# Kernel optimization log

Hardware: AMD Instinct MI355X
Metric: run time of the kernel (lower is better)

Reference implementation:

```python
import jax, jax.numpy as jnp
import numpy as np

DIM = 768
NUM_EXPERTS = 1536
EXPERT_DIM = 64
NOISE_SCALE = 0.1
B, H, W = 1, 64, 64
N = B * H * W


def setup_inputs() -> dict:
    key = jax.random.key(0)
    ks = jax.random.split(key, 6)
    scaled = lambda k, shape, fan_in: (jax.random.normal(k, shape, jnp.float32) / np.sqrt(fan_in)).astype(jnp.float32)
    return {
        "x": jax.random.normal(ks[0], (B, H, W, DIM), jnp.float32),
        "noise": jax.random.normal(ks[1], (N, NUM_EXPERTS), jnp.float32),
        "gate_w": scaled(ks[2], (NUM_EXPERTS, DIM), DIM),
        "gate_b": jnp.zeros((NUM_EXPERTS,), jnp.float32),
        "expert_w": scaled(ks[3], (NUM_EXPERTS, EXPERT_DIM, DIM), DIM),  # torch Linear weight layout (out, in)
        "expert_b": jnp.zeros((NUM_EXPERTS, EXPERT_DIM), jnp.float32),
        "proj_w": scaled(ks[4], (DIM, EXPERT_DIM), EXPERT_DIM),
        "proj_b": jnp.zeros((DIM,), jnp.float32),
    }


def reference(x, noise, gate_w, gate_b, expert_w, expert_b, proj_w, proj_b):
    orig_shape = x.shape
    xf = x.reshape(-1, orig_shape[-1])  # (N, DIM)
    # Noisy gating
    scores = xf @ gate_w.T + gate_b + noise * NOISE_SCALE  # (N, E)
    gate_weights = jax.nn.softmax(scores, axis=-1)
    top_w, top_i = jax.lax.top_k(gate_weights, 1)  # (N, 1), (N, 1)
    idx = top_i[:, 0]  # (N,)
    # Gather only the selected expert per token (same math as the redundant
    # dense all-expert compute followed by a gather in the original).
    w_sel = expert_w[idx]  # (N, EXPERT_DIM, DIM)
    b_sel = expert_b[idx]  # (N, EXPERT_DIM)
    y = jnp.einsum('nd,nod->no', xf, w_sel) + b_sel  # (N, EXPERT_DIM)
    out_flat = (y @ proj_w.T + proj_b) * top_w  # (N, DIM); top_w broadcasts (N,1)
    return out_flat.reshape(orig_shape)
```

## Files before the change

### kernel.cpp

```cpp
#include <hip/hip_runtime.h>
#include <hip/hip_bf16.h>

#define NT 4096
#define DIM 768
#define NE 1536
#define ED 64
#define GAP_THR 8e-3f

typedef __attribute__((ext_vector_type(8))) short short8v;
typedef __attribute__((ext_vector_type(4))) float f32x4;

__device__ __forceinline__ unsigned short f2bf(float f) {
  unsigned int u = __float_as_uint(f);
  unsigned int r = (u + 0x7fffu + ((u >> 16) & 1u)) >> 16;
  return (unsigned short)r;
}
__device__ __forceinline__ float bf2f(unsigned short h) {
  return __uint_as_float(((unsigned int)h) << 16);
}

__device__ __forceinline__ void gload16(const void* g, void* l) {
  __builtin_amdgcn_global_load_lds((const __attribute__((address_space(1))) void*)g,
                                   (__attribute__((address_space(3))) void*)l, 16, 0, 0);
}

__global__ __launch_bounds__(256) void split_bf16(
    const float* __restrict__ src, unsigned short* __restrict__ hi,
    unsigned short* __restrict__ lo, int n4) {
  int i = blockIdx.x * 256 + threadIdx.x;
  if (i >= n4) return;
  float4 v = ((const float4*)src)[i];
  unsigned short h0 = f2bf(v.x), h1 = f2bf(v.y), h2 = f2bf(v.z), h3 = f2bf(v.w);
  ushort4 hv = make_ushort4(h0, h1, h2, h3);
  ushort4 lv = make_ushort4(f2bf(v.x - bf2f(h0)), f2bf(v.y - bf2f(h1)),
                            f2bf(v.z - bf2f(h2)), f2bf(v.w - bf2f(h3)));
  ((ushort4*)hi)[i] = hv;
  ((ushort4*)lo)[i] = lv;
}

__global__ __launch_bounds__(256) void gate_mfma(
    const unsigned short* __restrict__ xhi, const unsigned short* __restrict__ xlo,
    const unsigned short* __restrict__ ghi, const unsigned short* __restrict__ glo,
    const float* __restrict__ gb, const float* __restrict__ noise,
    float* __restrict__ scores) {
  __shared__ __align__(16) unsigned short sA[2 * 128 * 32];
  __shared__ __align__(16) unsigned short sB[2 * 128 * 32];
  const int tid = threadIdx.x;
  const int w = tid >> 6, lane = tid & 63;
  const int wr = w >> 1, wc = w & 1;
  const int bm = blockIdx.x, bn = blockIdx.y;
  const int fr = lane & 15;
  const int fg = lane >> 4;
  const int gsw = fg ^ ((fr >> 1) & 3);

  f32x4 acc[4][4];
#pragma unroll
  for (int i = 0; i < 4; i++)
#pragma unroll
    for (int j = 0; j < 4; j++) acc[i][j] = (f32x4){0.f, 0.f, 0.f, 0.f};

  const size_t arow = (size_t)bm * 128 * DIM;
  const size_t brow = (size_t)bn * 128 * DIM;
  const int sr_lo = tid >> 2;
  const int sg = (tid & 3) ^ ((tid >> 3) & 3);

  for (int kt = 0; kt < DIM; kt += 32) {
    __syncthreads();
#pragma unroll
    for (int h = 0; h < 2; h++) {
      const int r = h * 64 + sr_lo;
      const size_t asrc = arow + (size_t)r * DIM + kt + sg * 8;
      const size_t bsrc = brow + (size_t)r * DIM + kt + sg * 8;
      const int dofs = h * 2048 + w * 512;
      gload16(xhi + asrc, &sA[dofs]);
      gload16(xlo + asrc, &sA[4096 + dofs]);
      gload16(ghi + bsrc, &sB[dofs]);
      gload16(glo + bsrc, &sB[4096 + dofs]);
    }
    __syncthreads();

    short8v ah[4], al[4], bh[4], bl[4];
#pragma unroll
    for (int mf = 0; mf < 4; mf++) {
      int ro = (wr * 64 + mf * 16 + fr) * 32 + gsw * 8;
      ah[mf] = *(const short8v*)&sA[ro];
      al[mf] = *(const short8v*)&sA[4096 + ro];
    }
#pragma unroll
    for (int nf = 0; nf < 4; nf++) {
      int ro = (wc * 64 + nf * 16 + fr) * 32 + gsw * 8;
      bh[nf] = *(const short8v*)&sB[ro];
      bl[nf] = *(const short8v*)&sB[4096 + ro];
    }
#pragma unroll
    for (int mf = 0; mf < 4; mf++)
#pragma unroll
      for (int nf = 0; nf < 4; nf++) {
        f32x4 c = acc[mf][nf];
        c = __builtin_amdgcn_mfma_f32_16x16x32_bf16(ah[mf], bh[nf], c, 0, 0, 0);
        c = __builtin_amdgcn_mfma_f32_16x16x32_bf16(ah[mf], bl[nf], c, 0, 0, 0);
        c = __builtin_amdgcn_mfma_f32_16x16x32_bf16(al[mf], bh[nf], c, 0, 0, 0);
        acc[mf][nf] = c;
      }
  }

  const int gm0 = bm * 128 + wr * 64;
  const int gn0 = bn * 128 + wc * 64;
#pragma unroll
  for (int nf = 0; nf < 4; nf++) {
    const int gn = gn0 + nf * 16 + fr;
    const float gbv = gb[gn];
#pragma unroll
    for (int mf = 0; mf < 4; mf++) {
      const int gmb = gm0 + mf * 16 + fg * 4;
#pragma unroll
      for (int reg = 0; reg < 4; reg++) {
        const size_t o = (size_t)(gmb + reg) * NE + gn;
        scores[o] = acc[mf][nf][reg] + gbv + 0.1f * noise[o];
      }
    }
  }
}

__global__ __launch_bounds__(256) void softmax_top1(
    const float* __restrict__ scores, float* __restrict__ topw,
    int* __restrict__ idx, int* __restrict__ rc_count,
    int* __restrict__ rc_n, int* __restrict__ rc_i2) {
  const int widx = threadIdx.x >> 6;
  const int lane = threadIdx.x & 63;
  const int n = blockIdx.x * 4 + widx;
  const float* s = scores + (size_t)n * NE;

  float v[24];
  float m1 = -1e30f, m2 = -1e30f;
  int i1 = 0, i2 = 0;
#pragma unroll
  for (int j = 0; j < 24; j++) {
    int ii = lane + 64 * j;
    v[j] = s[ii];
    if (v[j] > m1) { m2 = m1; i2 = i1; m1 = v[j]; i1 = ii; }
    else if (v[j] > m2) { m2 = v[j]; i2 = ii; }
  }
#pragma unroll
  for (int off = 32; off; off >>= 1) {
    float om1 = __shfl_xor(m1, off, 64); int oi1 = __shfl_xor(i1, off, 64);
    float om2 = __shfl_xor(m2, off, 64); int oi2 = __shfl_xor(i2, off, 64);
    if (om1 > m1 || (om1 == m1 && oi1 < i1)) {
      if (m1 > om2 || (m1 == om2 && i1 < oi2)) { m2 = m1; i2 = i1; }
      else { m2 = om2; i2 = oi2; }
      m1 = om1; i1 = oi1;
    } else {
      if (om1 > m2 || (om1 == m2 && oi1 < i2)) { m2 = om1; i2 = oi1; }
    }
  }
  float sum = 0.f;
#pragma unroll
  for (int j = 0; j < 24; j++) sum += __expf(v[j] - m1);
#pragma unroll
  for (int off = 32; off; off >>= 1) sum += __shfl_xor(sum, off, 64);

  if (lane == 0) {
    topw[n] = 1.0f / sum;
    idx[n] = i1;
    if (m1 - m2 < GAP_THR) {
      int p = atomicAdd(rc_count, 1);
      rc_n[p] = n; rc_i2[p] = i2;
    }
  }
}

__global__ __launch_bounds__(256) void recheck(
    const float* __restrict__ x, const float* __restrict__ gw,
    const float* __restrict__ gb, const float* __restrict__ noise,
    const int* __restrict__ rc_n, const int* __restrict__ rc_i2,
    const int* __restrict__ rc_count, int* __restrict__ idx) {
  __shared__ float r1[4], r2[4];
  const int cnt = *rc_count;
  const int tid = threadIdx.x;
  const int w = tid >> 6, lane = tid & 63;
  for (int t = blockIdx.x; t < cnt; t += gridDim.x) {
    const int n = rc_n[t];
    const int e1 = idx[n], e2 = rc_i2[t];
    const float* xr = x + (size_t)n * DIM;
    const float* w1 = gw + (size_t)e1 * DIM;
    const float* w2 = gw + (size_t)e2 * DIM;
    float p1 = 0.f, p2 = 0.f;
    for (int k = tid; k < DIM; k += 256) {
      float xv = xr[k];
      p1 += xv * w1[k];
      p2 += xv * w2[k];
    }
#pragma unroll
    for (int off = 32; off; off >>= 1) {
      p1 += __shfl_xor(p1, off, 64);
      p2 += __shfl_xor(p2, off, 64);
    }
    if (lane == 0) { r1[w] = p1; r2[w] = p2; }
    __syncthreads();
    if (tid == 0) {
      float s1 = r1[0] + r1[1] + r1[2] + r1[3] + gb[e1] + 0.1f * noise[(size_t)n * NE + e1];
      float s2 = r2[0] + r2[1] + r2[2] + r2[3] + gb[e2] + 0.1f * noise[(size_t)n * NE + e2];
      if (s2 > s1 || (s2 == s1 && e2 < e1)) idx[n] = e2;
    }
    __syncthreads();
  }
}

__global__ __launch_bounds__(256) void count_experts(
    const int* __restrict__ idx, int* __restrict__ counts) {
  const int n = blockIdx.x * 256 + threadIdx.x;
  atomicAdd(counts + idx[n], 1);
}

__global__ __launch_bounds__(256) void scan_offsets(
    const int* __restrict__ counts, int* __restrict__ offs, int* __restrict__ cursor) {
  __shared__ int part[256];
  const int t = threadIdx.x;
  int loc[6];
  int s = 0;
#pragma unroll
  for (int j = 0; j < 6; j++) { loc[j] = counts[t * 6 + j]; s += loc[j]; }
  part[t] = s;
  __syncthreads();
  for (int d = 1; d < 256; d <<= 1) {
    int v2 = (t >= d) ? part[t - d] : 0;
    __syncthreads();
    part[t] += v2;
    __syncthreads();
  }
  int excl = part[t] - s;
#pragma unroll
  for (int j = 0; j < 6; j++) {
    offs[t * 6 + j] = excl;
    cursor[t * 6 + j] = excl;
    excl += loc[j];
  }
}

__global__ __launch_bounds__(256) void scatter_tokens(
    const int* __restrict__ idx, int* __restrict__ cursor, int* __restrict__ sorted) {
  const int n = blockIdx.x * 256 + threadIdx.x;
  int e = idx[n];
  int pos = atomicAdd(cursor + e, 1);
  sorted[pos] = n;
}

__global__ __launch_bounds__(256) void expert_gemm(
    const float* __restrict__ x, const float* __restrict__ ew,
    const float* __restrict__ eb, const int* __restrict__ counts,
    const int* __restrict__ offs, const int* __restrict__ sorted,
    float* __restrict__ y) {
  const int e = blockIdx.x;
  const int cnt = counts[e];
  if (cnt == 0) return;
  const int base = offs[e];
  __shared__ float4 xs4[8 * 192];
  __shared__ int tok[8];
  const int tid = threadIdx.x;
  const int w = tid >> 6;
  const int lane = tid & 63;
  const float4* W4 = (const float4*)(ew + (size_t)e * ED * DIM);
  const float4* X4 = (const float4*)x;

  for (int c0 = 0; c0 < cnt; c0 += 8) {
    int cc = min(8, cnt - c0);
    __syncthreads();
    if (tid < cc) tok[tid] = sorted[base + c0 + tid];
    __syncthreads();
    int nf = cc * 192;
    for (int f = tid; f < nf; f += 256) {
      int t = f / 192, p = f % 192;
      xs4[t * 192 + p] = X4[(size_t)tok[t] * 192 + p];
    }
    __syncthreads();

    for (int oi = 0; oi < 16; oi++) {
      int o = w * 16 + oi;
      float4 w4a = W4[(size_t)o * 192 + lane];
      float4 w4b = W4[(size_t)o * 192 + lane + 64];
      float4 w4c = W4[(size_t)o * 192 + lane + 128];
      for (int t = 0; t < cc; t++) {
        float4 xa = xs4[t * 192 + lane];
        float4 xb = xs4[t * 192 + lane + 64];
        float4 xc = xs4[t * 192 + lane + 128];
        float p = w4a.x * xa.x + w4a.y * xa.y + w4a.z * xa.z + w4a.w * xa.w;
        p += w4b.x * xb.x + w4b.y * xb.y + w4b.z * xb.z + w4b.w * xb.w;
        p += w4c.x * xc.x + w4c.y * xc.y + w4c.z * xc.z + w4c.w * xc.w;
#pragma unroll
        for (int off = 32; off; off >>= 1) p += __shfl_xor(p, off, 64);
        if (lane == 0) y[(size_t)tok[t] * ED + o] = p + eb[e * ED + o];
      }
    }
  }
}

__global__ __launch_bounds__(256) void proj_kernel(
    const float* __restrict__ y, const float* __restrict__ pw,
    const float* __restrict__ pb, const float* __restrict__ topw,
    float* __restrict__ out) {
  const int b = blockIdx.x;
  const int tid = threadIdx.x;
  __shared__ float4 ys4[8 * 16];
  __shared__ float tw[8];
  if (tid < 128) {
    int t = tid >> 4, q = tid & 15;
    ys4[tid] = ((const float4*)y)[((size_t)b * 8 + t) * 16 + q];
  }
  if (tid < 8) tw[tid] = topw[b * 8 + tid];
  __syncthreads();
  const float4* pw4 = (const float4*)pw;
  for (int c = 0; c < 3; c++) {
    int d = c * 256 + tid;
    float4 pwv[16];
#pragma unroll
    for (int q = 0; q < 16; q++) pwv[q] = pw4[(size_t)d * 16 + q];
    float pbv = pb[d];
    for (int t = 0; t < 8; t++) {
      float s = 0.f;
#pragma unroll
      for (int q = 0; q < 16; q++) {
        float4 yv = ys4[t * 16 + q];
        s += pwv[q].x * yv.x + pwv[q].y * yv.y + pwv[q].z * yv.z + pwv[q].w * yv.w;
      }
      out[((size_t)b * 8 + t) * DIM + d] = (s + pbv) * tw[t];
    }
  }
}

extern "C" void kernel_launch(void* const* d_in, const int* in_sizes, int n_in,
                              void* d_out, int out_size, void* d_ws, size_t ws_size,
                              hipStream_t stream) {
  const float* x      = (const float*)d_in[0];
  const float* noise  = (const float*)d_in[1];
  const float* gate_w = (const float*)d_in[2];
  const float* gate_b = (const float*)d_in[3];
  const float* ew     = (const float*)d_in[4];
  const float* eb     = (const float*)d_in[5];
  const float* pw     = (const float*)d_in[6];
  const float* pb     = (const float*)d_in[7];
  float* out = (float*)d_out;

  char* ws = (char*)d_ws;
  float*          scores = (float*)(ws);
  unsigned short* xhi    = (unsigned short*)(ws + 25165824);
  unsigned short* xlo    = (unsigned short*)(ws + 31457280);
  unsigned short* ghi    = (unsigned short*)(ws + 37748736);
  unsigned short* glo    = (unsigned short*)(ws + 40108032);
  float*          y      = (float*)(ws + 42467328);
  float*          topw   = (float*)(ws + 43515904);
  int*            idx    = (int*)  (ws + 43532288);
  int*            counts = (int*)  (ws + 43548672);
  int*            rc_cnt = (int*)  (ws + 43554816);
  int*            offs   = (int*)  (ws + 43555072);
  int*            cursor = (int*)  (ws + 43561216);
  int*            sorted = (int*)  (ws + 43567360);
  int*            rc_n   = (int*)  (ws + 43583744);
  int*            rc_i2  = (int*)  (ws + 43600128);

  hipMemsetAsync(counts, 0, NE * sizeof(int) + 4, stream);

  split_bf16<<<NT * DIM / 4 / 256, 256, 0, stream>>>(x, xhi, xlo, NT * DIM / 4);
  split_bf16<<<NE * DIM / 4 / 256, 256, 0, stream>>>(gate_w, ghi, glo, NE * DIM / 4);
  gate_mfma<<<dim3(NT / 128, NE / 128), 256, 0, stream>>>(xhi, xlo, ghi, glo, gate_b, noise, scores);
  softmax_top1<<<NT / 4, 256, 0, stream>>>(scores, topw, idx, rc_cnt, rc_n, rc_i2);
  recheck<<<32, 256, 0, stream>>>(x, gate_w, gate_b, noise, rc_n, rc_i2, rc_cnt, idx);
  count_experts<<<NT / 256, 256, 0, stream>>>(idx, counts);
  scan_offsets<<<1, 256, 0, stream>>>(counts, offs, cursor);
  scatter_tokens<<<NT / 256, 256, 0, stream>>>(idx, cursor, sorted);
  expert_gemm<<<NE, 256, 0, stream>>>(x, ew, eb, counts, offs, sorted, y);
  proj_kernel<<<NT / 8, 256, 0, stream>>>(y, pw, pb, topw, out);
}
```

Before: 252.1 us.

## Fuse softmax/top-2 reduction into gate GEMM epilogue and merge split/count kernels

The gate GEMM epilogue now computes per-64-column partial top-2 and softmax partial sums in registers and writes small per-chunk partials, instead of writing the full 4096x1536 score matrix. A new finalize kernel merges the 24 partials per token with an online-softmax rescale and also counts experts with atomics, so the separate count kernel goes away. The recheck kernel adjusts counts when it flips a choice. The two bf16 split launches are merged into one. This removes a roughly 25 MB write and read of scores plus two launches, at the cost of extra shuffles in the GEMM epilogue.

After: 269.4 us. +6.9%, slower.

```diff
diff --git a/kernel.cpp b/kernel.cpp
--- a/kernel.cpp
+++ b/kernel.cpp
@@ -24,25 +24,39 @@
                                    (__attribute__((address_space(3))) void*)l, 16, 0, 0);
 }
 
-__global__ __launch_bounds__(256) void split_bf16(
-    const float* __restrict__ src, unsigned short* __restrict__ hi,
-    unsigned short* __restrict__ lo, int n4) {
+__device__ __forceinline__ void top2_merge(float& m1, int& i1, float& m2, int& i2,
+                                           float om1, int oi1, float om2, int oi2) {
+  if (om1 > m1 || (om1 == m1 && oi1 < i1)) {
+    if (m1 > om2 || (m1 == om2 && i1 < oi2)) { m2 = m1; i2 = i1; }
+    else { m2 = om2; i2 = oi2; }
+    m1 = om1; i1 = oi1;
+  } else {
+    if (om1 > m2 || (om1 == m2 && oi1 < i2)) { m2 = om1; i2 = oi1; }
+  }
+}
+
+__global__ __launch_bounds__(256) void split_all(
+    const float* __restrict__ x, const float* __restrict__ gw,
+    unsigned short* __restrict__ xhi, unsigned short* __restrict__ xlo,
+    unsigned short* __restrict__ ghi, unsigned short* __restrict__ glo) {
+  const int nx4 = NT * DIM / 4;
+  const int ng4 = NE * DIM / 4;
   int i = blockIdx.x * 256 + threadIdx.x;
-  if (i >= n4) return;
-  float4 v = ((const float4*)src)[i];
+  const float* src; unsigned short* hi; unsigned short* lo; int j;
+  if (i < nx4) { src = x; hi = xhi; lo = xlo; j = i; }
+  else { j = i - nx4; if (j >= ng4) return; src = gw; hi = ghi; lo = glo; }
+  float4 v = ((const float4*)src)[j];
   unsigned short h0 = f2bf(v.x), h1 = f2bf(v.y), h2 = f2bf(v.z), h3 = f2bf(v.w);
-  ushort4 hv = make_ushort4(h0, h1, h2, h3);
-  ushort4 lv = make_ushort4(f2bf(v.x - bf2f(h0)), f2bf(v.y - bf2f(h1)),
-                            f2bf(v.z - bf2f(h2)), f2bf(v.w - bf2f(h3)));
-  ((ushort4*)hi)[i] = hv;
-  ((ushort4*)lo)[i] = lv;
+  ((ushort4*)hi)[j] = make_ushort4(h0, h1, h2, h3);
+  ((ushort4*)lo)[j] = make_ushort4(f2bf(v.x - bf2f(h0)), f2bf(v.y - bf2f(h1)),
+                                   f2bf(v.z - bf2f(h2)), f2bf(v.w - bf2f(h3)));
 }
 
 __global__ __launch_bounds__(256) void gate_mfma(
     const unsigned short* __restrict__ xhi, const unsigned short* __restrict__ xlo,
     const unsigned short* __restrict__ ghi, const unsigned short* __restrict__ glo,
     const float* __restrict__ gb, const float* __restrict__ noise,
-    float* __restrict__ scores) {
+    float4* __restrict__ part_a, int* __restrict__ part_i2) {
   __shared__ __align__(16) unsigned short sA[2 * 128 * 32];
   __shared__ __align__(16) unsigned short sB[2 * 128 * 32];
   const int tid = threadIdx.x;
@@ -106,62 +120,77 @@
 
   const int gm0 = bm * 128 + wr * 64;
   const int gn0 = bn * 128 + wc * 64;
-#pragma unroll
-  for (int nf = 0; nf < 4; nf++) {
-    const int gn = gn0 + nf * 16 + fr;
-    const float gbv = gb[gn];
-#pragma unroll
-    for (int mf = 0; mf < 4; mf++) {
-      const int gmb = gm0 + mf * 16 + fg * 4;
+  const int chunk = bn * 2 + wc;
+  int gcol[4]; float gbv[4];
+#pragma unroll
+  for (int nf = 0; nf < 4; nf++) { gcol[nf] = gn0 + nf * 16 + fr; gbv[nf] = gb[gcol[nf]]; }
+#pragma unroll
+  for (int mf = 0; mf < 4; mf++) {
+    float sv[4][4];
+#pragma unroll
+    for (int nf = 0; nf < 4; nf++)
 #pragma unroll
       for (int reg = 0; reg < 4; reg++) {
-        const size_t o = (size_t)(gmb + reg) * NE + gn;
-        scores[o] = acc[mf][nf][reg] + gbv + 0.1f * noise[o];
-      }
-    }
-  }
-}
-
-__global__ __launch_bounds__(256) void softmax_top1(
-    const float* __restrict__ scores, float* __restrict__ topw,
-    int* __restrict__ idx, int* __restrict__ rc_count,
-    int* __restrict__ rc_n, int* __restrict__ rc_i2) {
-  const int widx = threadIdx.x >> 6;
-  const int lane = threadIdx.x & 63;
-  const int n = blockIdx.x * 4 + widx;
-  const float* s = scores + (size_t)n * NE;
-
-  float v[24];
-  float m1 = -1e30f, m2 = -1e30f;
-  int i1 = 0, i2 = 0;
-#pragma unroll
-  for (int j = 0; j < 24; j++) {
-    int ii = lane + 64 * j;
-    v[j] = s[ii];
-    if (v[j] > m1) { m2 = m1; i2 = i1; m1 = v[j]; i1 = ii; }
-    else if (v[j] > m2) { m2 = v[j]; i2 = ii; }
-  }
-#pragma unroll
-  for (int off = 32; off; off >>= 1) {
+        int gm = gm0 + mf * 16 + fg * 4 + reg;
+        sv[nf][reg] = acc[mf][nf][reg] + gbv[nf] + 0.1f * noise[(size_t)gm * NE + gcol[nf]];
+      }
+#pragma unroll
+    for (int reg = 0; reg < 4; reg++) {
+      float m1 = sv[0][reg]; int i1 = gcol[0];
+      float m2 = -3e38f; int i2 = 0x7fffffff;
+#pragma unroll
+      for (int nf = 1; nf < 4; nf++) {
+        float v = sv[nf][reg]; int ii = gcol[nf];
+        if (v > m1 || (v == m1 && ii < i1)) { m2 = m1; i2 = i1; m1 = v; i1 = ii; }
+        else if (v > m2 || (v == m2 && ii < i2)) { m2 = v; i2 = ii; }
+      }
+#pragma unroll
+      for (int off = 1; off <= 8; off <<= 1) {
+        float om1 = __shfl_xor(m1, off, 64); int oi1 = __shfl_xor(i1, off, 64);
+        float om2 = __shfl_xor(m2, off, 64); int oi2 = __shfl_xor(i2, off, 64);
+        top2_merge(m1, i1, m2, i2, om1, oi1, om2, oi2);
+      }
+      float ssum = 0.f;
+#pragma unroll
+      for (int nf = 0; nf < 4; nf++) ssum += __expf(sv[nf][reg] - m1);
+#pragma unroll
+      for (int off = 1; off <= 8; off <<= 1) ssum += __shfl_xor(ssum, off, 64);
+      if (fr == 0) {
+        int gm = gm0 + mf * 16 + fg * 4 + reg;
+        part_a[(size_t)gm * 24 + chunk] = make_float4(m1, m2, ssum, __int_as_float(i1));
+        part_i2[(size_t)gm * 24 + chunk] = i2;
+      }
+    }
+  }
+}
+
+__global__ __launch_bounds__(256) void finalize(
+    const float4* __restrict__ part_a, const int* __restrict__ part_i2,
+    float* __restrict__ topw, int* __restrict__ idx, int* __restrict__ counts,
+    int* __restrict__ rc_count, int* __restrict__ rc_n, int* __restrict__ rc_i2) {
+  const int wv = threadIdx.x >> 6, lane = threadIdx.x & 63;
+  const int n = blockIdx.x * 4 + wv;
+  float m1 = -3e38f, m2 = -3e38f, lm1 = -3e38f, lsum = 0.f;
+  int i1 = 0x7fffffff, i2 = 0x7fffffff;
+  if (lane < 24) {
+    float4 pa = part_a[(size_t)n * 24 + lane];
+    m1 = pa.x; m2 = pa.y; lsum = pa.z; i1 = __float_as_int(pa.w);
+    i2 = part_i2[(size_t)n * 24 + lane];
+    lm1 = pa.x;
+  }
+#pragma unroll
+  for (int off = 1; off <= 32; off <<= 1) {
     float om1 = __shfl_xor(m1, off, 64); int oi1 = __shfl_xor(i1, off, 64);
     float om2 = __shfl_xor(m2, off, 64); int oi2 = __shfl_xor(i2, off, 64);
-    if (om1 > m1 || (om1 == m1 && oi1 < i1)) {
-      if (m1 > om2 || (m1 == om2 && i1 < oi2)) { m2 = m1; i2 = i1; }
-      else { m2 = om2; i2 = oi2; }
-      m1 = om1; i1 = oi1;
-    } else {
-      if (om1 > m2 || (om1 == m2 && oi1 < i2)) { m2 = om1; i2 = oi1; }
-    }
-  }
-  float sum = 0.f;
-#pragma unroll
-  for (int j = 0; j < 24; j++) sum += __expf(v[j] - m1);
-#pragma unroll
-  for (int off = 32; off; off >>= 1) sum += __shfl_xor(sum, off, 64);
-
+    top2_merge(m1, i1, m2, i2, om1, oi1, om2, oi2);
+  }
+  float contrib = (lane < 24) ? __expf(lm1 - m1) * lsum : 0.f;
+#pragma unroll
+  for (int off = 1; off <= 32; off <<= 1) contrib += __shfl_xor(contrib, off, 64);
   if (lane == 0) {
-    topw[n] = 1.0f / sum;
+    topw[n] = 1.0f / contrib;
     idx[n] = i1;
+    atomicAdd(counts + i1, 1);
     if (m1 - m2 < GAP_THR) {
       int p = atomicAdd(rc_count, 1);
       rc_n[p] = n; rc_i2[p] = i2;
@@ -173,7 +202,7 @@
     const float* __restrict__ x, const float* __restrict__ gw,
     const float* __restrict__ gb, const float* __restrict__ noise,
     const int* __restrict__ rc_n, const int* __restrict__ rc_i2,
-    const int* __restrict__ rc_count, int* __restrict__ idx) {
+    const int* __restrict__ rc_count, int* __restrict__ idx, int* __restrict__ counts) {
   __shared__ float r1[4], r2[4];
   const int cnt = *rc_count;
   const int tid = threadIdx.x;
@@ -200,16 +229,14 @@
     if (tid == 0) {
       float s1 = r1[0] + r1[1] + r1[2] + r1[3] + gb[e1] + 0.1f * noise[(size_t)n * NE + e1];
       float s2 = r2[0] + r2[1] + r2[2] + r2[3] + gb[e2] + 0.1f * noise[(size_t)n * NE + e2];
-      if (s2 > s1 || (s2 == s1 && e2 < e1)) idx[n] = e2;
-    }
-    __syncthreads();
-  }
-}
-
-__global__ __launch_bounds__(256) void count_experts(
-    const int* __restrict__ idx, int* __restrict__ counts) {
-  const int n = blockIdx.x * 256 + threadIdx.x;
-  atomicAdd(counts + idx[n], 1);
+      if (s2 > s1 || (s2 == s1 && e2 < e1)) {
+        idx[n] = e2;
+        atomicSub(counts + e1, 1);
+        atomicAdd(counts + e2, 1);
+      }
+    }
+    __syncthreads();
+  }
 }
 
 __global__ __launch_bounds__(256) void scan_offsets(
@@ -341,30 +368,33 @@
   float* out = (float*)d_out;
 
   char* ws = (char*)d_ws;
-  float*          scores = (float*)(ws);
-  unsigned short* xhi    = (unsigned short*)(ws + 25165824);
-  unsigned short* xlo    = (unsigned short*)(ws + 31457280);
-  unsigned short* ghi    = (unsigned short*)(ws + 37748736);
-  unsigned short* glo    = (unsigned short*)(ws + 40108032);
-  float*          y      = (float*)(ws + 42467328);
-  float*          topw   = (float*)(ws + 43515904);
-  int*            idx    = (int*)  (ws + 43532288);
-  int*            counts = (int*)  (ws + 43548672);
-  int*            rc_cnt = (int*)  (ws + 43554816);
-  int*            offs   = (int*)  (ws + 43555072);
-  int*            cursor = (int*)  (ws + 43561216);
-  int*            sorted = (int*)  (ws + 43567360);
-  int*            rc_n   = (int*)  (ws + 43583744);
-  int*            rc_i2  = (int*)  (ws + 43600128);
+  unsigned short* xhi    = (unsigned short*)(ws);
+  unsigned short* xlo    = (unsigned short*)(ws + 6291456);
+  unsigned short* ghi    = (unsigned short*)(ws + 12582912);
+  unsigned short* glo    = (unsigned short*)(ws + 14942208);
+  float4*         part_a = (float4*)(ws + 17301504);
+  int*            part_i2= (int*)  (ws + 18874368);
+  float*          y      = (float*)(ws + 19267584);
+  float*          topw   = (float*)(ws + 20316160);
+  int*            idx    = (int*)  (ws + 20332544);
+  int*            counts = (int*)  (ws + 20348928);
+  int*            rc_cnt = (int*)  (ws + 20355072);
+  int*            offs   = (int*)  (ws + 20355328);
+  int*            cursor = (int*)  (ws + 20361472);
+  int*            sorted = (int*)  (ws + 20367616);
+  int*            rc_n   = (int*)  (ws + 20384000);
+  int*            rc_i2  = (int*)  (ws + 20400384);
 
   hipMemsetAsync(counts, 0, NE * sizeof(int) + 4, stream);
 
-  split_bf16<<<NT * DIM / 4 / 256, 256, 0, stream>>>(x, xhi, xlo, NT * DIM / 4);
-  split_bf16<<<NE * DIM / 4 / 256, 256, 0, stream>>>(gate_w, ghi, glo, NE * DIM / 4);
-  gate_mfma<<<dim3(NT / 128, NE / 128), 256, 0, stream>>>(xhi, xlo, ghi, glo, gate_b, noise, scores);
-  softmax_top1<<<NT / 4, 256, 0, stream>>>(scores, topw, idx, rc_cnt, rc_n, rc_i2);
-  recheck<<<32, 256, 0, stream>>>(x, gate_w, gate_b, noise, rc_n, rc_i2, rc_cnt, idx);
-  count_experts<<<NT / 256, 256, 0, stream>>>(idx, counts);
+  split_all<<<(NT * DIM / 4 + NE * DIM / 4 + 255) / 256, 256, 0, stream>>>(
+      x, gate_w, xhi, xlo, ghi, glo);
+  gate_mfma<<<dim3(NT / 128, NE / 128), 256, 0, stream>>>(
+      xhi, xlo, ghi, glo, gate_b, noise, part_a, part_i2);
+  finalize<<<NT / 4, 256, 0, stream>>>(part_a, part_i2, topw, idx, counts,
+                                       rc_cnt, rc_n, rc_i2);
+  recheck<<<32, 256, 0, stream>>>(x, gate_w, gate_b, noise, rc_n, rc_i2, rc_cnt,
+                                  idx, counts);
   scan_offsets<<<1, 256, 0, stream>>>(counts, offs, cursor);
   scatter_tokens<<<NT / 256, 256, 0, stream>>>(idx, cursor, sorted);
   expert_gemm<<<NE, 256, 0, stream>>>(x, ew, eb, counts, offs, sorted, y);
```
